# Optimization experiments

Measured on AMD Instinct MI355X. Metric: run time of the kernel, lower is better.

## Reference

```python
import jax, jax.numpy as jnp
import numpy as np
from jax import lax

B, D, K = 256, 128, 8192


def _conv_same(x, w, b):
    # x: [B,C,H,W], w: [O,I,3,3] (torch Conv2d layout), stride 1, padding 1 == SAME
    y = lax.conv_general_dilated(x, w, (1, 1), 'SAME',
                                 dimension_numbers=('NCHW', 'OIHW', 'NCHW'))
    return y + b[None, :, None, None]


def _convT_same(x, w, b):
    # torch ConvTranspose2d(k=3, stride=1, padding=1) with weight [I,O,3,3]
    # == SAME conv with spatially flipped kernel and swapped in/out channels
    wt = jnp.flip(w, axis=(2, 3)).transpose(1, 0, 2, 3)  # -> [O,I,3,3]
    return _conv_same(x, wt, b)


def setup_inputs() -> dict:
    key = jax.random.key(0)
    ks = jax.random.split(key, 12)
    s = 0.05
    return {
        'patch':  jax.random.normal(ks[0], (B, 3, 64, 64), jnp.float32),
        'enc_w1': jax.random.normal(ks[1], (64, 3, 3, 3), jnp.float32) * s,
        'enc_b1': jnp.zeros((64,), jnp.float32),
        'enc_w2': jax.random.normal(ks[2], (D, 64, 3, 3), jnp.float32) * s,
        'enc_b2': jnp.zeros((D,), jnp.float32),
        'emb':    jax.random.normal(ks[3], (K, D), jnp.float32),
        'dec_w1': jax.random.normal(ks[4], (D, 64, 3, 3), jnp.float32) * s,  # ConvT [in,out,k,k]
        'dec_b1': jnp.zeros((64,), jnp.float32),
        'dec_w2': jax.random.normal(ks[5], (64, 64, 3, 3), jnp.float32) * s,
        'dec_b2': jnp.zeros((64,), jnp.float32),
        'dec_w3': jax.random.normal(ks[6], (64, 3, 3, 3), jnp.float32) * s,
        'dec_b3': jnp.zeros((3,), jnp.float32),
    }


def reference(patch, enc_w1, enc_b1, enc_w2, enc_b2, emb,
              dec_w1, dec_b1, dec_w2, dec_b2, dec_w3, dec_b3):
    # ---- encode_patch ----
    h = jax.nn.relu(_conv_same(patch, enc_w1, enc_b1))
    h = _conv_same(h, enc_w2, enc_b2)
    z = jnp.mean(h, axis=(2, 3))  # AdaptiveAvgPool2d((1,1)) + flatten -> [B,D]

    # ---- VQ: cdist + argmin + gather ----
    # argmin over squared L2 == argmin over cdist(p=2); avoid sqrt.
    d2 = (jnp.sum(z * z, axis=1, keepdims=True)
          + jnp.sum(emb * emb, axis=1)[None, :]
          - 2.0 * z @ emb.T)  # [B,K]
    encoding_indices = jnp.argmin(d2, axis=1)  # [B]
    z_q = emb[encoding_indices]  # [B,D]

    commitment_loss = jnp.mean((lax.stop_gradient(z_q) - z) ** 2)
    codebook_loss = jnp.mean((z_q - lax.stop_gradient(z)) ** 2)

    # ---- decode_vector ----
    # bilinear interpolate of a 1x1 map to 64x64 is a pure broadcast
    v = jnp.broadcast_to(z_q[:, :, None, None], (z_q.shape[0], z_q.shape[1], 64, 64))
    d = jax.nn.relu(_convT_same(v, dec_w1, dec_b1))
    d = jax.nn.relu(_convT_same(d, dec_w2, dec_b2))
    recon = jnp.tanh(_convT_same(d, dec_w3, dec_b3))  # [B,3,64,64]

    return recon, codebook_loss, commitment_loss, encoding_indices[:, None]
```

## Files before the change

### kernel.cpp

```cpp
#include <hip/hip_runtime.h>
#include <math.h>


__global__ __launch_bounds__(256) void k_conv1_pre(
    const float* __restrict__ patch, const float* __restrict__ w1,
    const float* __restrict__ b1, const float* __restrict__ dw1,
    const float* __restrict__ emb, float* __restrict__ pstat,
    float* __restrict__ Wcfg, float* __restrict__ en2)
{
    __shared__ __align__(16) float lds[2304];
    const int blk = blockIdx.x;
    const int tid = threadIdx.x;

    if (blk >= 2048) {
        const int gid = (blk - 2048) * 256 + tid;
        if (gid < 73728) {
            const int cfg = gid >> 13;
            const int o = (gid >> 7) & 63;
            const int i = gid & 127;
            const int cy = cfg / 3, cx = cfg % 3;
            const int ylo = (cy == 2) ? 1 : 0, yhi = (cy == 0) ? 1 : 2;
            const int xlo = (cx == 2) ? 1 : 0, xhi = (cx == 0) ? 1 : 2;
            const float* wp = dw1 + ((size_t)i * 64 + o) * 9;
            float s = 0.f;
            for (int ky = ylo; ky <= yhi; ++ky)
                for (int kx = xlo; kx <= xhi; ++kx)
                    s += wp[ky * 3 + kx];
            Wcfg[gid] = s;
        } else if (gid < 81920) {
            const int k = gid - 73728;
            const float4* e = (const float4*)(emb + (size_t)k * 128);
            float s = 0.f;
            for (int t = 0; t < 32; ++t) {
                float4 v = e[t];
                s = fmaf(v.x, v.x, fmaf(v.y, v.y, fmaf(v.z, v.z, fmaf(v.w, v.w, s))));
            }
            en2[k] = s;
        }
        return;
    }

    const int b = blk >> 3, rg = blk & 7;
    const int y0 = rg * 8;
    const float* pb = patch + (size_t)b * 12288;
    for (int i = tid; i < 2160; i += 256) {
        const int c = i / 720, rem = i - c * 720;
        const int r = rem / 72, p = rem - r * 72;
        const int y = y0 + r - 1, x = p - 3;
        float v = 0.f;
        if (y >= 0 && y < 64 && x >= 0 && x < 64)
            v = pb[(c << 12) + (y << 6) + x];
        lds[i] = v;
    }
    __syncthreads();

    const int ch = tid & 63, q = tid >> 6;
    float w[3][3][3];
#pragma unroll
    for (int ic = 0; ic < 3; ++ic)
#pragma unroll
        for (int ky = 0; ky < 3; ++ky)
#pragma unroll
            for (int kx = 0; kx < 3; ++kx)
                w[ic][ky][kx] = w1[((ch * 3 + ic) * 3 + ky) * 3 + kx];
    const float bias = b1[ch];

    float T = 0, r0s = 0, r63s = 0, c0s = 0, c63s = 0;
    float h00 = 0, h063 = 0, h630 = 0, h6363 = 0;

#pragma unroll
    for (int sub = 0; sub < 2; ++sub) {
        const int yl = q * 2 + sub;
        const bool isr0  = (rg == 0) && (yl == 0);
        const bool isr63 = (rg == 7) && (yl == 7);
        float cr[3][3][2];
#pragma unroll
        for (int ic = 0; ic < 3; ++ic)
#pragma unroll
            for (int ky = 0; ky < 3; ++ky) {
                const float2 t2 = *(const float2*)&lds[(ic * 10 + yl + ky) * 72 + 2];
                cr[ic][ky][0] = t2.x; cr[ic][ky][1] = t2.y;
            }
#pragma unroll 4
        for (int xc = 0; xc < 16; ++xc) {
            float a0 = bias, a1 = bias, a2 = bias, a3 = bias;
#pragma unroll
            for (int ic = 0; ic < 3; ++ic)
#pragma unroll
                for (int ky = 0; ky < 3; ++ky) {
                    const float4 nw = *(const float4*)&lds[(ic * 10 + yl + ky) * 72 + xc * 4 + 4];
                    const float w0 = w[ic][ky][0], w1v = w[ic][ky][1], w2v = w[ic][ky][2];
                    a0 = fmaf(w0, cr[ic][ky][0], fmaf(w1v, cr[ic][ky][1], fmaf(w2v, nw.x, a0)));
                    a1 = fmaf(w0, cr[ic][ky][1], fmaf(w1v, nw.x, fmaf(w2v, nw.y, a1)));
                    a2 = fmaf(w0, nw.x, fmaf(w1v, nw.y, fmaf(w2v, nw.z, a2)));
                    a3 = fmaf(w0, nw.y, fmaf(w1v, nw.z, fmaf(w2v, nw.w, a3)));
                    cr[ic][ky][0] = nw.z; cr[ic][ky][1] = nw.w;
                }
            a0 = fmaxf(a0, 0.f); a1 = fmaxf(a1, 0.f);
            a2 = fmaxf(a2, 0.f); a3 = fmaxf(a3, 0.f);
            const float rs = (a0 + a1) + (a2 + a3);
            T += rs;
            if (isr0)  { r0s += rs;  if (xc == 0) h00 = a0;  if (xc == 15) h063 = a3; }
            if (isr63) { r63s += rs; if (xc == 0) h630 = a0; if (xc == 15) h6363 = a3; }
            if (xc == 0)  c0s += a0;
            if (xc == 15) c63s += a3;
        }
    }
    __syncthreads();
    float st[9] = {T, r0s, r63s, c0s, c63s, h00, h063, h630, h6363};
#pragma unroll
    for (int s = 0; s < 9; ++s) lds[(s * 4 + q) * 64 + ch] = st[s];
    __syncthreads();
    if (tid < 64) {
        float* pp = pstat + (size_t)blk * 576;
#pragma unroll
        for (int s = 0; s < 9; ++s)
            pp[s * 64 + tid] = lds[(s * 4 + 0) * 64 + tid] + lds[(s * 4 + 1) * 64 + tid]
                             + lds[(s * 4 + 2) * 64 + tid] + lds[(s * 4 + 3) * 64 + tid];
    }
}

__global__ __launch_bounds__(256) void k_zred(
    const float* __restrict__ pstat, const float* __restrict__ w2,
    const float* __restrict__ b2, float* __restrict__ z, float* __restrict__ zn2)
{
    __shared__ float fst[576];
    __shared__ __align__(16) float Ssh[576];
    __shared__ float zp[256];
    __shared__ float red2[128];
    const int b = blockIdx.x, tid = threadIdx.x;

    const float* pp = pstat + (size_t)b * 8 * 576;
    for (int i = tid; i < 576; i += 256) {
        float s = 0.f;
#pragma unroll
        for (int g = 0; g < 8; ++g) s += pp[g * 576 + i];
        fst[i] = s;
    }
    __syncthreads();

    if (tid < 64) {
        const int ch = tid;
        const float Tt   = fst[0 * 64 + ch], R0  = fst[1 * 64 + ch], R63 = fst[2 * 64 + ch];
        const float C0   = fst[3 * 64 + ch], C63 = fst[4 * 64 + ch];
        const float H00  = fst[5 * 64 + ch], H063 = fst[6 * 64 + ch];
        const float H630 = fst[7 * 64 + ch], H6363 = fst[8 * 64 + ch];
#pragma unroll
        for (int ky = 0; ky < 3; ++ky) {
            const float rex = (ky == 0) ? R63 : (ky == 2 ? R0 : 0.f);
#pragma unroll
            for (int kx = 0; kx < 3; ++kx) {
                const float cex = (kx == 0) ? C63 : (kx == 2 ? C0 : 0.f);
                float corner = 0.f;
                if (ky == 0 && kx == 0) corner = H6363;
                if (ky == 0 && kx == 2) corner = H630;
                if (ky == 2 && kx == 0) corner = H063;
                if (ky == 2 && kx == 2) corner = H00;
                Ssh[ch * 9 + ky * 3 + kx] = (Tt - rex - cex + corner) * (1.f / 4096.f);
            }
        }
    }
    __syncthreads();

    const int oc = tid & 127, h = tid >> 7;
    const float4* Wv = (const float4*)(w2 + (size_t)oc * 576 + h * 288);
    const float4* Sv = (const float4*)(Ssh + h * 288);
    float acc = 0.f;
    for (int t = 0; t < 72; ++t) {
        const float4 w4 = Wv[t], s4 = Sv[t];
        acc = fmaf(w4.x, s4.x, acc);
        acc = fmaf(w4.y, s4.y, acc);
        acc = fmaf(w4.z, s4.z, acc);
        acc = fmaf(w4.w, s4.w, acc);
    }
    zp[tid] = acc;
    __syncthreads();
    if (tid < 128) {
        const float zv = b2[tid] + zp[tid] + zp[tid + 128];
        z[(size_t)b * 128 + tid] = zv;
        red2[tid] = zv * zv;
    }
    __syncthreads();
    if (tid < 64) {
        float v = red2[tid] + red2[tid + 64];
        v += __shfl_xor(v, 32); v += __shfl_xor(v, 16); v += __shfl_xor(v, 8);
        v += __shfl_xor(v, 4);  v += __shfl_xor(v, 2);  v += __shfl_xor(v, 1);
        if (tid == 0) zn2[b] = v;
    }
}

__global__ __launch_bounds__(256) void k_vq(
    const float* __restrict__ z, const float* __restrict__ emb,
    const float* __restrict__ en2, float* __restrict__ pd2, int* __restrict__ pidx)
{
    __shared__ __align__(16) float zsh[2048];
    __shared__ float wd[16][4];
    __shared__ int   wi[16][4];
    const int tid = threadIdx.x;
    const int bg = blockIdx.x >> 4, kc = blockIdx.x & 15;
    const int b0 = bg * 16;
    for (int i = tid; i < 2048; i += 256) zsh[i] = z[(size_t)b0 * 128 + i];
    __syncthreads();

    const int k0 = kc * 512 + tid, k1 = k0 + 256;
    const float4* e0 = (const float4*)(emb + (size_t)k0 * 128);
    const float4* e1 = (const float4*)(emb + (size_t)k1 * 128);
    const float4* zv = (const float4*)zsh;

    float acc0[16], acc1[16];
#pragma unroll
    for (int bb = 0; bb < 16; ++bb) { acc0[bb] = 0.f; acc1[bb] = 0.f; }

    for (int t = 0; t < 32; ++t) {
        const float4 ea = e0[t], eb = e1[t];
#pragma unroll
        for (int bb = 0; bb < 16; ++bb) {
            const float4 zz = zv[bb * 32 + t];
            acc0[bb] = fmaf(zz.x, ea.x, fmaf(zz.y, ea.y, fmaf(zz.z, ea.z, fmaf(zz.w, ea.w, acc0[bb]))));
            acc1[bb] = fmaf(zz.x, eb.x, fmaf(zz.y, eb.y, fmaf(zz.z, eb.z, fmaf(zz.w, eb.w, acc1[bb]))));
        }
    }
    const float E0 = en2[k0], E1 = en2[k1];
    const int wv_ = tid >> 6, ln = tid & 63;
#pragma unroll
    for (int bb = 0; bb < 16; ++bb) {
        const float da = fmaf(-2.f, acc0[bb], E0);
        const float db = fmaf(-2.f, acc1[bb], E1);
        float d; int ix;
        if (da <= db) { d = da; ix = k0; } else { d = db; ix = k1; }
#pragma unroll
        for (int off = 32; off > 0; off >>= 1) {
            const float od = __shfl_xor(d, off);
            const int   oi = __shfl_xor(ix, off);
            if (od < d || (od == d && oi < ix)) { d = od; ix = oi; }
        }
        if (ln == 0) { wd[bb][wv_] = d; wi[bb][wv_] = ix; }
    }
    __syncthreads();
    if (tid < 16) {
        float d = wd[tid][0]; int ix = wi[tid][0];
#pragma unroll
        for (int wv2 = 1; wv2 < 4; ++wv2) {
            const float od = wd[tid][wv2]; const int oi = wi[tid][wv2];
            if (od < d || (od == d && oi < ix)) { d = od; ix = oi; }
        }
        pd2[(b0 + tid) * 16 + kc] = d;
        pidx[(b0 + tid) * 16 + kc] = ix;
    }
}

__global__ __launch_bounds__(256) void k_decode(
    const float* __restrict__ emb, const float* __restrict__ zn2,
    const float* __restrict__ pd2, const int* __restrict__ pidx,
    const float* __restrict__ Wcfg, const float* __restrict__ db1,
    const float* __restrict__ dw2, const float* __restrict__ db2,
    const float* __restrict__ dw3, const float* __restrict__ db3,
    float* __restrict__ out)
{
    __shared__ __align__(16) float zsh[128];
    __shared__ float d1e[64][10];
    __shared__ float d2e[64][26];
    __shared__ float o3[3 * 49];
    __shared__ int   bisld[256];
    __shared__ float redl[256];

    const int b = blockIdx.x, tid = threadIdx.x;

    float dmin = pd2[tid * 16]; int bi = pidx[tid * 16];
    for (int j = 1; j < 16; ++j) {
        const float d = pd2[tid * 16 + j]; const int ix = pidx[tid * 16 + j];
        if (d < dmin || (d == dmin && ix < bi)) { dmin = d; bi = ix; }
    }
    bisld[tid] = bi;
    redl[tid] = dmin + zn2[tid];
    __syncthreads();

    const int mybi = bisld[b];
    if (tid < 128) { zsh[tid] = emb[(size_t)mybi * 128 + tid]; redl[tid] += redl[tid + 128]; }
    if (tid >= 128 && tid < 192) { d1e[tid - 128][9] = 0.f; d2e[tid - 128][25] = 0.f; }
    __syncthreads();
    if (tid < 64) {
        float v = redl[tid] + redl[tid + 64];
        v += __shfl_xor(v, 32); v += __shfl_xor(v, 16); v += __shfl_xor(v, 8);
        v += __shfl_xor(v, 4);  v += __shfl_xor(v, 2);  v += __shfl_xor(v, 1);
        if (tid == 0 && b == 0) {
            const float L = v * (1.f / 32768.f);
            out[3145728] = L;
            out[3145729] = L;
        }
    }
    if (b == 0) out[3145730 + tid] = (float)bisld[tid];

    for (int id = tid; id < 576; id += 256) {
        const int o = id / 9, cfg = id % 9;
        const float4* wv = (const float4*)(Wcfg + ((size_t)cfg * 64 + o) * 128);
        const float4* zv = (const float4*)zsh;
        float acc = db1[o];
        for (int t = 0; t < 32; ++t) {
            const float4 w4 = wv[t], z4 = zv[t];
            acc = fmaf(w4.x, z4.x, acc);
            acc = fmaf(w4.y, z4.y, acc);
            acc = fmaf(w4.z, z4.z, acc);
            acc = fmaf(w4.w, z4.w, acc);
        }
        d1e[o][cfg] = fmaxf(acc, 0.f);
    }
    __syncthreads();

    {
        const int TY5[5][3] = {{-1,0,1},{0,1,1},{1,1,1},{1,1,2},{1,2,-1}};
        const int o = tid >> 2, isub = tid & 3;
        float acc[25];
#pragma unroll
        for (int c = 0; c < 25; ++c) acc[c] = 0.f;
        for (int ii = 0; ii < 16; ++ii) {
            const int i = isub + ii * 4;
            float d1v[10];
#pragma unroll
            for (int t = 0; t < 9; ++t) d1v[t] = d1e[i][t];
            d1v[9] = 0.f;
            float w9[9];
            const float* wp = dw2 + ((size_t)i * 64 + o) * 9;
#pragma unroll
            for (int t = 0; t < 9; ++t) w9[t] = wp[t];
#pragma unroll
            for (int cy = 0; cy < 5; ++cy) {
#pragma unroll
                for (int ky = 0; ky < 3; ++ky) {
                    const int ty = TY5[cy][ky];
                    if (ty < 0) continue;
#pragma unroll
                    for (int cx = 0; cx < 5; ++cx) {
#pragma unroll
                        for (int kx = 0; kx < 3; ++kx) {
                            const int tx = TY5[cx][kx];
                            if (tx < 0) continue;
                            acc[cy * 5 + cx] = fmaf(w9[(2 - ky) * 3 + (2 - kx)],
                                                    d1v[ty * 3 + tx], acc[cy * 5 + cx]);
                        }
                    }
                }
            }
        }
#pragma unroll
        for (int c = 0; c < 25; ++c) {
            float v = acc[c];
            v += __shfl_xor(v, 1);
            v += __shfl_xor(v, 2);
            if (isub == 0) d2e[o][c] = fmaxf(v + db2[o], 0.f);
        }
    }
    __syncthreads();

    if (tid < 147) {
        const int TY7[7][3] = {{-1,0,1},{0,1,2},{1,2,2},{2,2,2},{2,2,3},{2,3,4},{3,4,-1}};
        const int c3 = tid / 49, cc = tid % 49, cy = cc / 7, cx = cc % 7;
        float acc = db3[c3];
        for (int i = 0; i < 64; ++i) {
            const float* wp = dw3 + ((size_t)i * 3 + c3) * 9;
#pragma unroll
            for (int ky = 0; ky < 3; ++ky) {
                const int ty = TY7[cy][ky];
#pragma unroll
                for (int kx = 0; kx < 3; ++kx) {
                    const int tx = TY7[cx][kx];
                    const int t = (ty < 0 || tx < 0) ? 25 : ty * 5 + tx;
                    acc = fmaf(wp[(2 - ky) * 3 + (2 - kx)], d2e[i][t], acc);
                }
            }
        }
        o3[c3 * 49 + cc] = tanhf(acc);
    }
    __syncthreads();

    float4* ob = (float4*)(out + (size_t)b * 12288);
    for (int id = tid; id < 3072; id += 256) {
        const int base = id * 4;
        const int c = base >> 12, rem = base & 4095, y = rem >> 6, x0 = rem & 63;
        const int ry = (y <= 3) ? y : (y >= 60 ? y - 57 : 3);
        const float* row = &o3[c * 49 + ry * 7];
        float4 v;
        int x;
        x = x0 + 0; v.x = row[(x <= 3) ? x : (x >= 60 ? x - 57 : 3)];
        x = x0 + 1; v.y = row[(x <= 3) ? x : (x >= 60 ? x - 57 : 3)];
        x = x0 + 2; v.z = row[(x <= 3) ? x : (x >= 60 ? x - 57 : 3)];
        x = x0 + 3; v.w = row[(x <= 3) ? x : (x >= 60 ? x - 57 : 3)];
        ob[id] = v;
    }
}

extern "C" void kernel_launch(void* const* d_in, const int* in_sizes, int n_in,
                              void* d_out, int out_size, void* d_ws, size_t ws_size,
                              hipStream_t stream)
{
    const float* patch  = (const float*)d_in[0];
    const float* enc_w1 = (const float*)d_in[1];
    const float* enc_b1 = (const float*)d_in[2];
    const float* enc_w2 = (const float*)d_in[3];
    const float* enc_b2 = (const float*)d_in[4];
    const float* emb    = (const float*)d_in[5];
    const float* dec_w1 = (const float*)d_in[6];
    const float* dec_b1 = (const float*)d_in[7];
    const float* dec_w2 = (const float*)d_in[8];
    const float* dec_b2 = (const float*)d_in[9];
    const float* dec_w3 = (const float*)d_in[10];
    const float* dec_b3 = (const float*)d_in[11];

    float* out = (float*)d_out;
    float* ws  = (float*)d_ws;

    float* pstat = ws;
    float* z     = ws + 1179648;
    float* zn2   = ws + 1212416;
    float* pd2   = ws + 1212672;
    int*   pidx  = (int*)(ws + 1216768);
    float* Wcfg  = ws + 1220864;
    float* en2   = ws + 1294592;

    k_conv1_pre<<<dim3(2368), dim3(256), 0, stream>>>(patch, enc_w1, enc_b1, dec_w1,
                                                      emb, pstat, Wcfg, en2);
    k_zred<<<dim3(256), dim3(256), 0, stream>>>(pstat, enc_w2, enc_b2, z, zn2);
    k_vq<<<dim3(256), dim3(256), 0, stream>>>(z, emb, en2, pd2, pidx);
    k_decode<<<dim3(256), dim3(256), 0, stream>>>(emb, zn2, pd2, pidx, Wcfg, dec_b1,
                                                  dec_w2, dec_b2, dec_w3, dec_b3, out);
}
```

Measured before the change: 131.3 us.

## Fuse encoder conv and z-reduction per image, split decoder stage1 into batched kernel

The first conv and the z reduction now run in one kernel with one 512-thread block per image that holds the whole padded patch in LDS. This removes the pstat round trip and the separate k_zred launch, at the cost of far fewer, heavier blocks. The VQ kernel now uses 8 batch rows per block instead of 16, doubling its grid. A new stage1 kernel computes the first decoder layer for groups of 8 images from an LDS-staged weight slab. The decode kernel also caches dw3 in LDS and uses vector loads for dw2.

```diff
diff --git a/kernel.cpp b/kernel.cpp
--- a/kernel.cpp
+++ b/kernel.cpp
@@ -1,19 +1,22 @@
 #include <hip/hip_runtime.h>
 #include <math.h>
 
-
-__global__ __launch_bounds__(256) void k_conv1_pre(
+typedef float float4u __attribute__((ext_vector_type(4), aligned(4)));
+
+
+__global__ __launch_bounds__(512) void k_conv_z(
     const float* __restrict__ patch, const float* __restrict__ w1,
-    const float* __restrict__ b1, const float* __restrict__ dw1,
-    const float* __restrict__ emb, float* __restrict__ pstat,
+    const float* __restrict__ b1, const float* __restrict__ w2,
+    const float* __restrict__ b2, const float* __restrict__ dw1,
+    const float* __restrict__ emb,
+    float* __restrict__ z, float* __restrict__ zn2,
     float* __restrict__ Wcfg, float* __restrict__ en2)
 {
-    __shared__ __align__(16) float lds[2304];
-    const int blk = blockIdx.x;
-    const int tid = threadIdx.x;
-
-    if (blk >= 2048) {
-        const int gid = (blk - 2048) * 256 + tid;
+    __shared__ __align__(16) float lds[14256];
+    const int blk = blockIdx.x, tid = threadIdx.x;
+
+    if (blk >= 256) {
+        const int gid = (blk - 256) * 512 + tid;
         if (gid < 73728) {
             const int cfg = gid >> 13;
             const int o = (gid >> 7) & 63;
@@ -27,12 +30,12 @@
                 for (int kx = xlo; kx <= xhi; ++kx)
                     s += wp[ky * 3 + kx];
             Wcfg[gid] = s;
-        } else if (gid < 81920) {
+        } else {
             const int k = gid - 73728;
             const float4* e = (const float4*)(emb + (size_t)k * 128);
             float s = 0.f;
             for (int t = 0; t < 32; ++t) {
-                float4 v = e[t];
+                const float4 v = e[t];
                 s = fmaf(v.x, v.x, fmaf(v.y, v.y, fmaf(v.z, v.z, fmaf(v.w, v.w, s))));
             }
             en2[k] = s;
@@ -40,13 +43,11 @@
         return;
     }
 
-    const int b = blk >> 3, rg = blk & 7;
-    const int y0 = rg * 8;
-    const float* pb = patch + (size_t)b * 12288;
-    for (int i = tid; i < 2160; i += 256) {
-        const int c = i / 720, rem = i - c * 720;
+    const float* pb = patch + (size_t)blk * 12288;
+    for (int i = tid; i < 14256; i += 512) {
+        const int c = i / 4752, rem = i - c * 4752;
         const int r = rem / 72, p = rem - r * 72;
-        const int y = y0 + r - 1, x = p - 3;
+        const int y = r - 1, x = p - 3;
         float v = 0.f;
         if (y >= 0 && y < 64 && x >= 0 && x < 64)
             v = pb[(c << 12) + (y << 6) + x];
@@ -68,83 +69,60 @@
     float T = 0, r0s = 0, r63s = 0, c0s = 0, c63s = 0;
     float h00 = 0, h063 = 0, h630 = 0, h6363 = 0;
 
-#pragma unroll
-    for (int sub = 0; sub < 2; ++sub) {
-        const int yl = q * 2 + sub;
-        const bool isr0  = (rg == 0) && (yl == 0);
-        const bool isr63 = (rg == 7) && (yl == 7);
-        float cr[3][3][2];
-#pragma unroll
-        for (int ic = 0; ic < 3; ++ic)
-#pragma unroll
-            for (int ky = 0; ky < 3; ++ky) {
-                const float2 t2 = *(const float2*)&lds[(ic * 10 + yl + ky) * 72 + 2];
-                cr[ic][ky][0] = t2.x; cr[ic][ky][1] = t2.y;
-            }
-#pragma unroll 4
-        for (int xc = 0; xc < 16; ++xc) {
-            float a0 = bias, a1 = bias, a2 = bias, a3 = bias;
+#pragma unroll 1
+    for (int r8 = 0; r8 < 8; ++r8) {
+        const int y = q * 8 + r8;
+#pragma unroll 1
+        for (int m = 0; m < 8; ++m) {
+            float a[8];
+#pragma unroll
+            for (int j = 0; j < 8; ++j) a[j] = bias;
 #pragma unroll
             for (int ic = 0; ic < 3; ++ic)
 #pragma unroll
                 for (int ky = 0; ky < 3; ++ky) {
-                    const float4 nw = *(const float4*)&lds[(ic * 10 + yl + ky) * 72 + xc * 4 + 4];
+                    const float* rowp = &lds[(ic * 66 + y + ky) * 72 + m * 8 + 2];
+                    const float2 f01 = *(const float2*)rowp;
+                    const float4 f25 = *(const float4*)(rowp + 2);
+                    const float4 f69 = *(const float4*)(rowp + 6);
+                    const float f[10] = {f01.x, f01.y, f25.x, f25.y, f25.z, f25.w,
+                                         f69.x, f69.y, f69.z, f69.w};
                     const float w0 = w[ic][ky][0], w1v = w[ic][ky][1], w2v = w[ic][ky][2];
-                    a0 = fmaf(w0, cr[ic][ky][0], fmaf(w1v, cr[ic][ky][1], fmaf(w2v, nw.x, a0)));
-                    a1 = fmaf(w0, cr[ic][ky][1], fmaf(w1v, nw.x, fmaf(w2v, nw.y, a1)));
-                    a2 = fmaf(w0, nw.x, fmaf(w1v, nw.y, fmaf(w2v, nw.z, a2)));
-                    a3 = fmaf(w0, nw.y, fmaf(w1v, nw.z, fmaf(w2v, nw.w, a3)));
-                    cr[ic][ky][0] = nw.z; cr[ic][ky][1] = nw.w;
+#pragma unroll
+                    for (int j = 0; j < 8; ++j)
+                        a[j] = fmaf(w0, f[j], fmaf(w1v, f[j + 1], fmaf(w2v, f[j + 2], a[j])));
                 }
-            a0 = fmaxf(a0, 0.f); a1 = fmaxf(a1, 0.f);
-            a2 = fmaxf(a2, 0.f); a3 = fmaxf(a3, 0.f);
-            const float rs = (a0 + a1) + (a2 + a3);
+#pragma unroll
+            for (int j = 0; j < 8; ++j) a[j] = fmaxf(a[j], 0.f);
+            const float rs = ((a[0] + a[1]) + (a[2] + a[3])) + ((a[4] + a[5]) + (a[6] + a[7]));
             T += rs;
-            if (isr0)  { r0s += rs;  if (xc == 0) h00 = a0;  if (xc == 15) h063 = a3; }
-            if (isr63) { r63s += rs; if (xc == 0) h630 = a0; if (xc == 15) h6363 = a3; }
-            if (xc == 0)  c0s += a0;
-            if (xc == 15) c63s += a3;
-        }
-    }
-    __syncthreads();
-    float st[9] = {T, r0s, r63s, c0s, c63s, h00, h063, h630, h6363};
-#pragma unroll
-    for (int s = 0; s < 9; ++s) lds[(s * 4 + q) * 64 + ch] = st[s];
-    __syncthreads();
+            if (y == 0)  { r0s += rs;  if (m == 0) h00 = a[0];  if (m == 7) h063 = a[7]; }
+            if (y == 63) { r63s += rs; if (m == 0) h630 = a[0]; if (m == 7) h6363 = a[7]; }
+            if (m == 0) c0s += a[0];
+            if (m == 7) c63s += a[7];
+        }
+    }
+    __syncthreads();
+
+    {
+        const float st[9] = {T, r0s, r63s, c0s, c63s, h00, h063, h630, h6363};
+#pragma unroll
+        for (int s = 0; s < 9; ++s) lds[(s * 8 + q) * 64 + ch] = st[s];
+    }
+    __syncthreads();
+
+    float* Ssh = lds + 4608;
     if (tid < 64) {
-        float* pp = pstat + (size_t)blk * 576;
-#pragma unroll
-        for (int s = 0; s < 9; ++s)
-            pp[s * 64 + tid] = lds[(s * 4 + 0) * 64 + tid] + lds[(s * 4 + 1) * 64 + tid]
-                             + lds[(s * 4 + 2) * 64 + tid] + lds[(s * 4 + 3) * 64 + tid];
-    }
-}
-
-__global__ __launch_bounds__(256) void k_zred(
-    const float* __restrict__ pstat, const float* __restrict__ w2,
-    const float* __restrict__ b2, float* __restrict__ z, float* __restrict__ zn2)
-{
-    __shared__ float fst[576];
-    __shared__ __align__(16) float Ssh[576];
-    __shared__ float zp[256];
-    __shared__ float red2[128];
-    const int b = blockIdx.x, tid = threadIdx.x;
-
-    const float* pp = pstat + (size_t)b * 8 * 576;
-    for (int i = tid; i < 576; i += 256) {
-        float s = 0.f;
-#pragma unroll
-        for (int g = 0; g < 8; ++g) s += pp[g * 576 + i];
-        fst[i] = s;
-    }
-    __syncthreads();
-
-    if (tid < 64) {
-        const int ch = tid;
-        const float Tt   = fst[0 * 64 + ch], R0  = fst[1 * 64 + ch], R63 = fst[2 * 64 + ch];
-        const float C0   = fst[3 * 64 + ch], C63 = fst[4 * 64 + ch];
-        const float H00  = fst[5 * 64 + ch], H063 = fst[6 * 64 + ch];
-        const float H630 = fst[7 * 64 + ch], H6363 = fst[8 * 64 + ch];
+        float f[9];
+#pragma unroll
+        for (int s = 0; s < 9; ++s) {
+            float v = 0.f;
+#pragma unroll
+            for (int g = 0; g < 8; ++g) v += lds[(s * 8 + g) * 64 + tid];
+            f[s] = v;
+        }
+        const float Tt = f[0], R0 = f[1], R63 = f[2], C0 = f[3], C63 = f[4];
+        const float H00 = f[5], H063 = f[6], H630 = f[7], H6363 = f[8];
 #pragma unroll
         for (int ky = 0; ky < 3; ++ky) {
             const float rex = (ky == 0) ? R63 : (ky == 2 ? R0 : 0.f);
@@ -156,28 +134,32 @@
                 if (ky == 0 && kx == 2) corner = H630;
                 if (ky == 2 && kx == 0) corner = H063;
                 if (ky == 2 && kx == 2) corner = H00;
-                Ssh[ch * 9 + ky * 3 + kx] = (Tt - rex - cex + corner) * (1.f / 4096.f);
+                Ssh[tid * 9 + ky * 3 + kx] = (Tt - rex - cex + corner) * (1.f / 4096.f);
             }
         }
     }
     __syncthreads();
 
-    const int oc = tid & 127, h = tid >> 7;
-    const float4* Wv = (const float4*)(w2 + (size_t)oc * 576 + h * 288);
-    const float4* Sv = (const float4*)(Ssh + h * 288);
-    float acc = 0.f;
-    for (int t = 0; t < 72; ++t) {
-        const float4 w4 = Wv[t], s4 = Sv[t];
-        acc = fmaf(w4.x, s4.x, acc);
-        acc = fmaf(w4.y, s4.y, acc);
-        acc = fmaf(w4.z, s4.z, acc);
-        acc = fmaf(w4.w, s4.w, acc);
-    }
-    zp[tid] = acc;
-    __syncthreads();
+    float* zp = lds + 5184;
+    {
+        const int oc = tid & 127, h = tid >> 7;
+        const float4* Wv = (const float4*)(w2 + (size_t)oc * 576 + h * 144);
+        const float4* Sv = (const float4*)(Ssh + h * 144);
+        float acc = 0.f;
+        for (int t = 0; t < 36; ++t) {
+            const float4 w4 = Wv[t], s4 = Sv[t];
+            acc = fmaf(w4.x, s4.x, acc);
+            acc = fmaf(w4.y, s4.y, acc);
+            acc = fmaf(w4.z, s4.z, acc);
+            acc = fmaf(w4.w, s4.w, acc);
+        }
+        zp[tid] = acc;
+    }
+    __syncthreads();
+    float* red2 = lds + 5696;
     if (tid < 128) {
-        const float zv = b2[tid] + zp[tid] + zp[tid + 128];
-        z[(size_t)b * 128 + tid] = zv;
+        const float zv = b2[tid] + ((zp[tid] + zp[tid + 128]) + (zp[tid + 256] + zp[tid + 384]));
+        z[(size_t)blk * 128 + tid] = zv;
         red2[tid] = zv * zv;
     }
     __syncthreads();
@@ -185,7 +167,7 @@
         float v = red2[tid] + red2[tid + 64];
         v += __shfl_xor(v, 32); v += __shfl_xor(v, 16); v += __shfl_xor(v, 8);
         v += __shfl_xor(v, 4);  v += __shfl_xor(v, 2);  v += __shfl_xor(v, 1);
-        if (tid == 0) zn2[b] = v;
+        if (tid == 0) zn2[blk] = v;
     }
 }
 
@@ -193,13 +175,13 @@
     const float* __restrict__ z, const float* __restrict__ emb,
     const float* __restrict__ en2, float* __restrict__ pd2, int* __restrict__ pidx)
 {
-    __shared__ __align__(16) float zsh[2048];
-    __shared__ float wd[16][4];
-    __shared__ int   wi[16][4];
+    __shared__ __align__(16) float zsh[1024];
+    __shared__ float wd[8][4];
+    __shared__ int   wi[8][4];
     const int tid = threadIdx.x;
     const int bg = blockIdx.x >> 4, kc = blockIdx.x & 15;
-    const int b0 = bg * 16;
-    for (int i = tid; i < 2048; i += 256) zsh[i] = z[(size_t)b0 * 128 + i];
+    const int b0 = bg * 8;
+    for (int i = tid; i < 1024; i += 256) zsh[i] = z[(size_t)b0 * 128 + i];
     __syncthreads();
 
     const int k0 = kc * 512 + tid, k1 = k0 + 256;
@@ -207,14 +189,14 @@
     const float4* e1 = (const float4*)(emb + (size_t)k1 * 128);
     const float4* zv = (const float4*)zsh;
 
-    float acc0[16], acc1[16];
-#pragma unroll
-    for (int bb = 0; bb < 16; ++bb) { acc0[bb] = 0.f; acc1[bb] = 0.f; }
+    float acc0[8], acc1[8];
+#pragma unroll
+    for (int bb = 0; bb < 8; ++bb) { acc0[bb] = 0.f; acc1[bb] = 0.f; }
 
     for (int t = 0; t < 32; ++t) {
         const float4 ea = e0[t], eb = e1[t];
 #pragma unroll
-        for (int bb = 0; bb < 16; ++bb) {
+        for (int bb = 0; bb < 8; ++bb) {
             const float4 zz = zv[bb * 32 + t];
             acc0[bb] = fmaf(zz.x, ea.x, fmaf(zz.y, ea.y, fmaf(zz.z, ea.z, fmaf(zz.w, ea.w, acc0[bb]))));
             acc1[bb] = fmaf(zz.x, eb.x, fmaf(zz.y, eb.y, fmaf(zz.z, eb.z, fmaf(zz.w, eb.w, acc1[bb]))));
@@ -223,7 +205,7 @@
     const float E0 = en2[k0], E1 = en2[k1];
     const int wv_ = tid >> 6, ln = tid & 63;
 #pragma unroll
-    for (int bb = 0; bb < 16; ++bb) {
+    for (int bb = 0; bb < 8; ++bb) {
         const float da = fmaf(-2.f, acc0[bb], E0);
         const float db = fmaf(-2.f, acc1[bb], E1);
         float d; int ix;
@@ -237,7 +219,7 @@
         if (ln == 0) { wd[bb][wv_] = d; wi[bb][wv_] = ix; }
     }
     __syncthreads();
-    if (tid < 16) {
+    if (tid < 8) {
         float d = wd[tid][0]; int ix = wi[tid][0];
 #pragma unroll
         for (int wv2 = 1; wv2 < 4; ++wv2) {
@@ -249,52 +231,60 @@
     }
 }
 
-__global__ __launch_bounds__(256) void k_decode(
+__global__ __launch_bounds__(256) void k_stage1(
     const float* __restrict__ emb, const float* __restrict__ zn2,
     const float* __restrict__ pd2, const int* __restrict__ pidx,
     const float* __restrict__ Wcfg, const float* __restrict__ db1,
-    const float* __restrict__ dw2, const float* __restrict__ db2,
-    const float* __restrict__ dw3, const float* __restrict__ db3,
-    float* __restrict__ out)
+    float* __restrict__ d1all, float* __restrict__ out)
 {
-    __shared__ __align__(16) float zsh[128];
-    __shared__ float d1e[64][10];
-    __shared__ float d2e[64][26];
-    __shared__ float o3[3 * 49];
-    __shared__ int   bisld[256];
+    __shared__ float wsl[64 * 132];
+    __shared__ float zql[8 * 132];
+    __shared__ int   bish[8];
     __shared__ float redl[256];
-
-    const int b = blockIdx.x, tid = threadIdx.x;
+    const int tid = threadIdx.x;
+    const int g = blockIdx.x / 9, c = blockIdx.x - g * 9;
+    const int b0 = g * 8;
 
     float dmin = pd2[tid * 16]; int bi = pidx[tid * 16];
     for (int j = 1; j < 16; ++j) {
         const float d = pd2[tid * 16 + j]; const int ix = pidx[tid * 16 + j];
         if (d < dmin || (d == dmin && ix < bi)) { dmin = d; bi = ix; }
     }
-    bisld[tid] = bi;
+    if (tid >= b0 && tid < b0 + 8) bish[tid - b0] = bi;
     redl[tid] = dmin + zn2[tid];
     __syncthreads();
-
-    const int mybi = bisld[b];
-    if (tid < 128) { zsh[tid] = emb[(size_t)mybi * 128 + tid]; redl[tid] += redl[tid + 128]; }
-    if (tid >= 128 && tid < 192) { d1e[tid - 128][9] = 0.f; d2e[tid - 128][25] = 0.f; }
+    if (blockIdx.x == 0) out[3145730 + tid] = (float)bi;
+    if (tid < 128) redl[tid] += redl[tid + 128];
     __syncthreads();
     if (tid < 64) {
         float v = redl[tid] + redl[tid + 64];
         v += __shfl_xor(v, 32); v += __shfl_xor(v, 16); v += __shfl_xor(v, 8);
         v += __shfl_xor(v, 4);  v += __shfl_xor(v, 2);  v += __shfl_xor(v, 1);
-        if (tid == 0 && b == 0) {
+        if (tid == 0 && blockIdx.x == 0) {
             const float L = v * (1.f / 32768.f);
             out[3145728] = L;
             out[3145729] = L;
         }
     }
-    if (b == 0) out[3145730 + tid] = (float)bisld[tid];
-
-    for (int id = tid; id < 576; id += 256) {
-        const int o = id / 9, cfg = id % 9;
-        const float4* wv = (const float4*)(Wcfg + ((size_t)cfg * 64 + o) * 128);
-        const float4* zv = (const float4*)zsh;
+
+    for (int idx = tid; idx < 2048; idx += 256) {
+        const int o = idx >> 5, k4 = idx & 31;
+        *(float4*)&wsl[o * 132 + k4 * 4] =
+            *(const float4*)&Wcfg[((size_t)c * 64 + o) * 128 + k4 * 4];
+    }
+    {
+        const int b = tid >> 5, k4 = tid & 31;
+        *(float4*)&zql[b * 132 + k4 * 4] =
+            *(const float4*)&emb[(size_t)bish[b] * 128 + k4 * 4];
+    }
+    __syncthreads();
+
+#pragma unroll
+    for (int pp = 0; pp < 2; ++pp) {
+        const int pair = tid + pp * 256;
+        const int o = pair >> 3, bb = pair & 7;
+        const float4* wv = (const float4*)&wsl[o * 132];
+        const float4* zv = (const float4*)&zql[bb * 132];
         float acc = db1[o];
         for (int t = 0; t < 32; ++t) {
             const float4 w4 = wv[t], z4 = zv[t];
@@ -303,8 +293,24 @@
             acc = fmaf(w4.z, z4.z, acc);
             acc = fmaf(w4.w, z4.w, acc);
         }
-        d1e[o][cfg] = fmaxf(acc, 0.f);
-    }
+        d1all[((size_t)(b0 + bb)) * 576 + o * 9 + c] = fmaxf(acc, 0.f);
+    }
+}
+
+__global__ __launch_bounds__(256) void k_decode(
+    const float* __restrict__ d1all, const float* __restrict__ dw2,
+    const float* __restrict__ db2, const float* __restrict__ dw3,
+    const float* __restrict__ db3, float* __restrict__ out)
+{
+    __shared__ float d1e[64][10];
+    __shared__ float d2e[64][26];
+    __shared__ float o3[3 * 49];
+    __shared__ float dw3sh[1728];
+
+    const int b = blockIdx.x, tid = threadIdx.x;
+    for (int id = tid; id < 576; id += 256) d1e[id / 9][id % 9] = d1all[(size_t)b * 576 + id];
+    for (int id = tid; id < 1728; id += 256) dw3sh[id] = dw3[id];
+    if (tid < 64) { d1e[tid][9] = 0.f; d2e[tid][25] = 0.f; }
     __syncthreads();
 
     {
@@ -312,17 +318,18 @@
         const int o = tid >> 2, isub = tid & 3;
         float acc[25];
 #pragma unroll
-        for (int c = 0; c < 25; ++c) acc[c] = 0.f;
+        for (int cc = 0; cc < 25; ++cc) acc[cc] = 0.f;
         for (int ii = 0; ii < 16; ++ii) {
             const int i = isub + ii * 4;
             float d1v[10];
 #pragma unroll
             for (int t = 0; t < 9; ++t) d1v[t] = d1e[i][t];
             d1v[9] = 0.f;
-            float w9[9];
             const float* wp = dw2 + ((size_t)i * 64 + o) * 9;
-#pragma unroll
-            for (int t = 0; t < 9; ++t) w9[t] = wp[t];
+            const float4u w03 = *(const float4u*)wp;
+            const float4u w47 = *(const float4u*)(wp + 4);
+            const float w8v = wp[8];
+            const float w9[9] = {w03.x, w03.y, w03.z, w03.w, w47.x, w47.y, w47.z, w47.w, w8v};
 #pragma unroll
             for (int cy = 0; cy < 5; ++cy) {
 #pragma unroll
@@ -343,11 +350,11 @@
             }
         }
 #pragma unroll
-        for (int c = 0; c < 25; ++c) {
-            float v = acc[c];
+        for (int cc = 0; cc < 25; ++cc) {
+            float v = acc[cc];
             v += __shfl_xor(v, 1);
             v += __shfl_xor(v, 2);
-            if (isub == 0) d2e[o][c] = fmaxf(v + db2[o], 0.f);
+            if (isub == 0) d2e[o][cc] = fmaxf(v + db2[o], 0.f);
         }
     }
     __syncthreads();
@@ -357,7 +364,7 @@
         const int c3 = tid / 49, cc = tid % 49, cy = cc / 7, cx = cc % 7;
         float acc = db3[c3];
         for (int i = 0; i < 64; ++i) {
-            const float* wp = dw3 + ((size_t)i * 3 + c3) * 9;
+            const float* wp = &dw3sh[(i * 3 + c3) * 9];
 #pragma unroll
             for (int ky = 0; ky < 3; ++ky) {
                 const int ty = TY7[cy][ky];
@@ -409,18 +416,19 @@
     float* out = (float*)d_out;
     float* ws  = (float*)d_ws;
 
-    float* pstat = ws;
-    float* z     = ws + 1179648;
-    float* zn2   = ws + 1212416;
-    float* pd2   = ws + 1212672;
-    int*   pidx  = (int*)(ws + 1216768);
-    float* Wcfg  = ws + 1220864;
-    float* en2   = ws + 1294592;
-
-    k_conv1_pre<<<dim3(2368), dim3(256), 0, stream>>>(patch, enc_w1, enc_b1, dec_w1,
-                                                      emb, pstat, Wcfg, en2);
-    k_zred<<<dim3(256), dim3(256), 0, stream>>>(pstat, enc_w2, enc_b2, z, zn2);
-    k_vq<<<dim3(256), dim3(256), 0, stream>>>(z, emb, en2, pd2, pidx);
-    k_decode<<<dim3(256), dim3(256), 0, stream>>>(emb, zn2, pd2, pidx, Wcfg, dec_b1,
-                                                  dec_w2, dec_b2, dec_w3, dec_b3, out);
+    float* z     = ws;
+    float* zn2   = ws + 32768;
+    float* pd2   = ws + 33024;
+    int*   pidx  = (int*)(ws + 37120);
+    float* Wcfg  = ws + 41216;
+    float* en2   = ws + 114944;
+    float* d1all = ws + 123136;
+
+    k_conv_z<<<dim3(416), dim3(512), 0, stream>>>(patch, enc_w1, enc_b1, enc_w2, enc_b2,
+                                                  dec_w1, emb, z, zn2, Wcfg, en2);
+    k_vq<<<dim3(512), dim3(256), 0, stream>>>(z, emb, en2, pd2, pidx);
+    k_stage1<<<dim3(288), dim3(256), 0, stream>>>(emb, zn2, pd2, pidx, Wcfg, dec_b1,
+                                                  d1all, out);
+    k_decode<<<dim3(256), dim3(256), 0, stream>>>(d1all, dec_w2, dec_b2, dec_w3,
+                                                  dec_b3, out);
 }
```

New measurement: 146.8 us. 11.8% more time.
